# Kernel optimization log

Hardware: AMD Instinct MI355X
Metric: run time of the kernel (lower is better)

The kernel has to match this reference:

```python
import jax, jax.numpy as jnp
import numpy as np

EPS = 1e-5

def _conv1x1_bn(x, W, b, g, beta):
    # 1x1 conv == channel matmul; BN in training mode uses batch stats over (N,H,W)
    y = jnp.einsum('bchw,oc->bohw', x, W) + b[None, :, None, None]
    mu = jnp.mean(y, axis=(0, 2, 3))
    var = jnp.var(y, axis=(0, 2, 3))
    y = (y - mu[None, :, None, None]) * jax.lax.rsqrt(var + EPS)[None, :, None, None]
    return y * g[None, :, None, None] + beta[None, :, None, None]


def setup_inputs() -> dict:
    key = jax.random.key(0)
    ks = jax.random.split(key, 7)
    b, c, h, w = 8, 256, 64, 64
    sc = 1.0 / np.sqrt(c)
    inp = {
        'x': jax.random.normal(ks[0], (b, c, h, w), jnp.float32),
        'Wq': jax.random.normal(ks[1], (c, c), jnp.float32) * sc,
        'bq': jax.random.normal(ks[2], (c,), jnp.float32) * 0.02,
        'gq': jnp.ones((c,), jnp.float32),
        'betaq': jnp.zeros((c,), jnp.float32),
        'Wk': jax.random.normal(ks[3], (c, c), jnp.float32) * sc,
        'bk': jax.random.normal(ks[4], (c,), jnp.float32) * 0.02,
        'gk': jnp.ones((c,), jnp.float32),
        'betak': jnp.zeros((c,), jnp.float32),
        'Wv': jax.random.normal(ks[5], (c, c), jnp.float32) * sc,
        'bv': jax.random.normal(ks[6], (c,), jnp.float32) * 0.02,
        'gv': jnp.ones((c,), jnp.float32),
        'betav': jnp.zeros((c,), jnp.float32),
    }
    return inp


def reference(x, Wq, bq, gq, betaq, Wk, bk, gk, betak, Wv, bv, gv, betav):
    b, c, h, w = x.shape
    scale = float(h) ** (-0.5)
    Q = _conv1x1_bn(x, Wq, bq, gq, betaq).reshape(b, c, h * w)
    K = _conv1x1_bn(x, Wk, bk, gk, betak).reshape(b, c, h * w)
    V = _conv1x1_bn(x, Wv, bv, gv, betav).reshape(b, c, h * w)
    # un-normalized attention (no softmax)
    pixelMap = jnp.einsum('bcq,bck->bqk', Q, K) * scale  # [b, N, N]
    out = jnp.einsum('bqk,bck->bcq', pixelMap, V)        # [b, c, N]
    return out.reshape(b, c, h, w)
```

## Files before the change

### kernel.cpp

```cpp
#include <hip/hip_runtime.h>
#include <hip/hip_bf16.h>


#define BB 8
#define CC 256
#define NPIX 4096
#define PTOT 32768
#define EPSV 1e-5f
#define SCALEV 0.125f

#define OFF_PG    0L
#define OFF_SP    6291456L
#define OFF_S     6324224L
#define OFF_GHAT  6326272L
#define OFF_XBAR  6391808L
#define OFF_WP    6392064L
#define OFF_WKTF  6588672L
#define OFF_WVTF  6654208L
#define OFF_CVEC  6719744L
#define OFF_U     6720512L
#define OFF_HB    6722560L
#define OFF_R     6724608L
#define OFF_OFFV  6724864L
#define OFF_GBF   6726912L
#define OFF_WQT   6989056L
#define OFF_WKT   7021824L
#define OFF_WVB   7054592L
#define OFF_ZT    7087360L
#define OFF_TBF   7120128L

typedef __attribute__((ext_vector_type(8))) short short8;
typedef __attribute__((ext_vector_type(4))) float f32x4;

#define MFMA16(a, b, c) __builtin_amdgcn_mfma_f32_16x16x32_bf16((a), (b), (c), 0, 0, 0)

__device__ __forceinline__ ushort f2bf(float f) {
    union { float f; unsigned u; } v; v.f = f;
    const unsigned r = (v.u + 0x7FFFu + ((v.u >> 16) & 1u)) >> 16;
    return (ushort)r;
}

__device__ __forceinline__ float bf2f(ushort u) {
    union { unsigned u; float f; } v; v.u = ((unsigned)u) << 16;
    return v.f;
}

__device__ __forceinline__ ushort2 f2bf2(float a, float b) {
    __hip_bfloat162 h = __float22bfloat162_rn(float2{a, b});
    union { __hip_bfloat162 h; ushort2 u; } v; v.h = h;
    return v.u;
}

__device__ __forceinline__ float block_reduce(float v, float* red, int tid) {
    red[tid] = v; __syncthreads();
    for (int st = 128; st > 0; st >>= 1) {
        if (tid < st) red[tid] += red[tid + st];
        __syncthreads();
    }
    float r = red[0]; __syncthreads();
    return r;
}

__device__ __forceinline__ float2 wred2(float a, float b, float* red8, int tid) {
    #pragma unroll
    for (int s = 32; s > 0; s >>= 1) {
        a += __shfl_xor(a, s);
        b += __shfl_xor(b, s);
    }
    if ((tid & 63) == 0) { red8[(tid >> 6) * 2] = a; red8[(tid >> 6) * 2 + 1] = b; }
    __syncthreads();
    const float ra = red8[0] + red8[2] + red8[4] + red8[6];
    const float rb = red8[1] + red8[3] + red8[5] + red8[7];
    __syncthreads();
    return float2{ra, rb};
}

__global__ __launch_bounds__(256, 2) void gram_mfma(const float* __restrict__ x,
                                                    float* __restrict__ Pg,
                                                    float* __restrict__ Sp,
                                                    float* __restrict__ Ghat) {
    __shared__ __align__(16) ushort Ab[128 * 72];
    __shared__ __align__(16) ushort Bb[128 * 72];
    __shared__ float rs[128];
    const int tid = threadIdx.x;
    const int ks = blockIdx.x, b = blockIdx.y, tt = blockIdx.z;
    const int lb = (tt * 8 + b) * 16 + ks;
    if (lb < 64) {
        #pragma unroll
        for (int i = 0; i < 4; ++i) Ghat[lb * 1024 + i * 256 + tid] = 0.f;
    }
    const int it = (tt == 1) ? 1 : 0;
    const int jt = (tt == 0) ? 0 : 1;
    const bool diag = (tt < 2);
    const int i0 = it * 128, j0 = jt * 128, k0 = ks * 256;
    const float* xb = x + (long)b * CC * NPIX;
    const int c = tid & 15, rp = tid >> 4;
    const int wave = tid >> 6, lane = tid & 63;
    const int wr = (wave >> 1) * 64, wc = (wave & 1) * 64;
    const int m = lane & 15, q8 = (lane >> 4) * 8;

    if (tid < 128) rs[tid] = 0.f;
    float rloc[8] = {};
    f32x4 acc[4][4];
    #pragma unroll
    for (int a = 0; a < 4; ++a)
        #pragma unroll
        for (int q = 0; q < 4; ++q) acc[a][q] = (f32x4){0.f, 0.f, 0.f, 0.f};

    const float* Abase = xb + (long)i0 * NPIX + k0 + c * 4;
    const float* Bbase = xb + (long)j0 * NPIX + k0 + c * 4;

    float4 va[8], vb[8];
    #pragma unroll
    for (int pp = 0; pp < 8; ++pp)
        va[pp] = *(const float4*)&Abase[(long)(pp * 16 + rp) * NPIX];
    if (!diag) {
        #pragma unroll
        for (int pp = 0; pp < 8; ++pp)
            vb[pp] = *(const float4*)&Bbase[(long)(pp * 16 + rp) * NPIX];
    }

    for (int kc = 0; kc < 256; kc += 64) {
        __syncthreads();
        #pragma unroll
        for (int pp = 0; pp < 8; ++pp) {
            const int row = pp * 16 + rp;
            const float4 v = va[pp];
            rloc[pp] += v.x + v.y + v.z + v.w;
            const ushort2 w01 = f2bf2(v.x, v.y);
            const ushort2 w23 = f2bf2(v.z, v.w);
            ushort4 w; w.x = w01.x; w.y = w01.y; w.z = w23.x; w.w = w23.y;
            *(ushort4*)&Ab[row * 72 + c * 4] = w;
        }
        if (!diag) {
            #pragma unroll
            for (int pp = 0; pp < 8; ++pp) {
                const int row = pp * 16 + rp;
                const float4 v = vb[pp];
                const ushort2 w01 = f2bf2(v.x, v.y);
                const ushort2 w23 = f2bf2(v.z, v.w);
                ushort4 w; w.x = w01.x; w.y = w01.y; w.z = w23.x; w.w = w23.y;
                *(ushort4*)&Bb[row * 72 + c * 4] = w;
            }
        }
        const int kn = kc + 64;
        if (kn < 256) {
            #pragma unroll
            for (int pp = 0; pp < 8; ++pp)
                va[pp] = *(const float4*)&Abase[(long)(pp * 16 + rp) * NPIX + kn];
            if (!diag) {
                #pragma unroll
                for (int pp = 0; pp < 8; ++pp)
                    vb[pp] = *(const float4*)&Bbase[(long)(pp * 16 + rp) * NPIX + kn];
            }
        }
        __syncthreads();
        const ushort* Bsrc = diag ? Ab : Bb;
        #pragma unroll
        for (int kk = 0; kk < 2; ++kk) {
            short8 af[4], bfv[4];
            #pragma unroll
            for (int a = 0; a < 4; ++a)
                af[a] = *(const short8*)&Ab[(wr + a * 16 + m) * 72 + kk * 32 + q8];
            #pragma unroll
            for (int q = 0; q < 4; ++q)
                bfv[q] = *(const short8*)&Bsrc[(wc + q * 16 + m) * 72 + kk * 32 + q8];
            #pragma unroll
            for (int a = 0; a < 4; ++a)
                #pragma unroll
                for (int q = 0; q < 4; ++q)
                    acc[a][q] = MFMA16(af[a], bfv[q], acc[a][q]);
        }
    }
    if (diag) {
        #pragma unroll
        for (int pp = 0; pp < 8; ++pp) atomicAdd(&rs[pp * 16 + rp], rloc[pp]);
        __syncthreads();
        if (tid < 128) Sp[(((long)ks * 8 + b) * 2 + it) * 128 + tid] = rs[tid];
    }
    float* Pt = Pg + (((long)ks * 8 + b) * 3 + tt) * 16384;
    const int rq = (lane >> 4) * 4;
    #pragma unroll
    for (int a = 0; a < 4; ++a) {
        #pragma unroll
        for (int q = 0; q < 4; ++q) {
            const int col = wc + q * 16 + m;
            #pragma unroll
            for (int reg = 0; reg < 4; ++reg)
                Pt[(long)(wr + a * 16 + rq + reg) * 128 + col] = acc[a][q][reg];
        }
    }
}

__global__ __launch_bounds__(256) void reduce_mirror(const float* __restrict__ Pg,
                                                     const float* __restrict__ Sp,
                                                     ushort* __restrict__ Gbf,
                                                     float* __restrict__ Ghat,
                                                     float* __restrict__ S,
                                                     float* __restrict__ xbar) {
    const int blk = blockIdx.x, tid = threadIdx.x;
    if (blk == 384) {
        const int it2 = tid >> 7, rr = tid & 127;
        float xacc = 0.f;
        for (int b = 0; b < BB; ++b) {
            float acc = 0.f;
            #pragma unroll
            for (int ks = 0; ks < 16; ++ks)
                acc += Sp[(((long)ks * 8 + b) * 2 + it2) * 128 + rr];
            S[b * 256 + tid] = acc;
            xacc += acc;
        }
        xbar[tid] = xacc * (1.0f / PTOT);
        return;
    }
    __shared__ float tile[32][33];
    const int tt = blk >> 7;
    const int sub = (blk >> 3) & 15;
    const int b = blk & 7;
    const int sr = (sub >> 2) * 32, sc = (sub & 3) * 32;
    const int it = (tt == 1) ? 1 : 0;
    const int jt = (tt == 0) ? 0 : 1;
    const bool offd = (tt == 2);
    const int gi0 = it * 128 + sr, gj0 = jt * 128 + sc;
    const int r = tid >> 3, c4 = (tid & 7) * 4;
    const float inv = 1.0f / PTOT;

    float s0 = 0.f, s1 = 0.f, s2 = 0.f, s3 = 0.f;
    #pragma unroll
    for (int ks = 0; ks < 16; ++ks) {
        const float4 v = *(const float4*)&Pg[(((long)ks * 8 + b) * 3 + tt) * 16384
                                             + (long)(sr + r) * 128 + sc + c4];
        s0 += v.x; s1 += v.y; s2 += v.z; s3 += v.w;
    }
    ushort4 w;
    w.x = f2bf(s0); w.y = f2bf(s1); w.z = f2bf(s2); w.w = f2bf(s3);
    *(ushort4*)&Gbf[(long)b * 65536 + (long)(gi0 + r) * 256 + gj0 + c4] = w;
    float* gd = &Ghat[(long)(gi0 + r) * 256 + gj0 + c4];
    atomicAdd(gd + 0, s0 * inv);
    atomicAdd(gd + 1, s1 * inv);
    atomicAdd(gd + 2, s2 * inv);
    atomicAdd(gd + 3, s3 * inv);
    if (offd) {
        tile[r][c4 + 0] = s0; tile[r][c4 + 1] = s1;
        tile[r][c4 + 2] = s2; tile[r][c4 + 3] = s3;
        __syncthreads();
        const float t0 = tile[c4 + 0][r], t1 = tile[c4 + 1][r];
        const float t2 = tile[c4 + 2][r], t3 = tile[c4 + 3][r];
        ushort4 tw;
        tw.x = f2bf(t0); tw.y = f2bf(t1); tw.z = f2bf(t2); tw.w = f2bf(t3);
        *(ushort4*)&Gbf[(long)b * 65536 + (long)(gj0 + r) * 256 + gi0 + c4] = tw;
        float* gm = &Ghat[(long)(gj0 + r) * 256 + gi0 + c4];
        atomicAdd(gm + 0, t0 * inv);
        atomicAdd(gm + 1, t1 * inv);
        atomicAdd(gm + 2, t2 * inv);
        atomicAdd(gm + 3, t3 * inv);
    }
}

__global__ __launch_bounds__(256) void stats_quad(const float* __restrict__ Wq, const float* __restrict__ Wk,
                           const float* __restrict__ Wv, const float* __restrict__ Ghat,
                           const float* __restrict__ xbar,
                           const float* bq, const float* gq, const float* betaq,
                           const float* bk, const float* gk, const float* betak,
                           const float* bv, const float* gv, const float* betav,
                           float* __restrict__ Wp, float* __restrict__ cvec,
                           ushort* __restrict__ WqT, ushort* __restrict__ WkT,
                           ushort* __restrict__ Wvb, float* __restrict__ WkTf,
                           float* __restrict__ WvTf) {
    const int og = blockIdx.x, t = blockIdx.y, tid = threadIdx.x;
    const int o0 = og * 4;
    const float* Wt  = t == 0 ? Wq : (t == 1 ? Wk : Wv);
    const float* bt  = t == 0 ? bq : (t == 1 ? bk : bv);
    const float* gt  = t == 0 ? gq : (t == 1 ? gk : gv);
    const float* bet = t == 0 ? betaq : (t == 1 ? betak : betav);
    __shared__ float wrows[4][256];
    __shared__ float red8[8];
    #pragma unroll
    for (int i = 0; i < 4; ++i) wrows[i][tid] = Wt[(o0 + i) * 256 + tid];
    const float xb = xbar[tid];
    __syncthreads();
    const float* grow = Ghat + (long)tid * 256;
    float tj[4] = {0.f, 0.f, 0.f, 0.f};
    #pragma unroll 8
    for (int k = 0; k < 256; k += 4) {
        const float4 g = *(const float4*)&grow[k];
        #pragma unroll
        for (int i = 0; i < 4; ++i)
            tj[i] += g.x * wrows[i][k]     + g.y * wrows[i][k + 1]
                   + g.z * wrows[i][k + 2] + g.w * wrows[i][k + 3];
    }
    #pragma unroll
    for (int i = 0; i < 4; ++i) {
        const int o = o0 + i;
        const float wv = wrows[i][tid];
        const float2 qw = wred2(wv * tj[i], wv * xb, red8, tid);
        const float bo = bt[o];
        const float mu = qw.y + bo;
        const float var = qw.x + 2.f * bo * mu - bo * bo - mu * mu;
        const float a = gt[o] * rsqrtf(var + EPSV);
        const float wpv = a * wv;
        Wp[(long)t * 65536 + o * 256 + tid] = wpv;
        const ushort wb = f2bf(wpv);
        if (t == 0) {
            WqT[(long)tid * 256 + o] = wb;
        } else if (t == 1) {
            WkT[(long)tid * 256 + o] = wb;
            WkTf[(long)tid * 256 + o] = wpv;
        } else {
            Wvb[(long)o * 256 + tid] = wb;
            WvTf[(long)tid * 256 + o] = wpv;
        }
        if (tid == 0) cvec[t * 256 + o] = a * (bo - mu) + bet[o];
    }
}

__device__ __forceinline__ void gemm_tile0(const ushort* __restrict__ Ab,
                                           const ushort* __restrict__ Bb,
                                           ushort* __restrict__ Db,
                                           int m0, int n0, int tid) {
    const int wave = tid >> 6, lane = tid & 63;
    const int wr = (wave >> 1) * 64, wc = (wave & 1) * 64;
    const int m = lane & 15, q8 = (lane >> 4) * 8;
    f32x4 acc[4][4];
    #pragma unroll
    for (int a = 0; a < 4; ++a)
        #pragma unroll
        for (int q = 0; q < 4; ++q) acc[a][q] = (f32x4){0.f, 0.f, 0.f, 0.f};
    #pragma unroll
    for (int kk = 0; kk < 8; ++kk) {
        short8 af[4], bfv[4];
        #pragma unroll
        for (int a = 0; a < 4; ++a)
            af[a] = *(const short8*)&Ab[(long)(m0 + wr + a * 16 + m) * 256 + kk * 32 + q8];
        #pragma unroll
        for (int q = 0; q < 4; ++q)
            bfv[q] = *(const short8*)&Bb[(long)(n0 + wc + q * 16 + m) * 256 + kk * 32 + q8];
        #pragma unroll
        for (int a = 0; a < 4; ++a)
            #pragma unroll
            for (int q = 0; q < 4; ++q)
                acc[a][q] = MFMA16(af[a], bfv[q], acc[a][q]);
    }
    const int rq = (lane >> 4) * 4;
    #pragma unroll
    for (int a = 0; a < 4; ++a) {
        #pragma unroll
        for (int q = 0; q < 4; ++q) {
            const int col = n0 + wc + q * 16 + m;
            #pragma unroll
            for (int reg = 0; reg < 4; ++reg)
                Db[(long)col * 256 + (m0 + wr + a * 16 + rq + reg)] = f2bf(acc[a][q][reg]);
        }
    }
}

__global__ __launch_bounds__(256) void zmidabc(const ushort* __restrict__ WkT,
                                               const ushort* __restrict__ WqT,
                                               ushort* __restrict__ ZT,
                                               const float* __restrict__ Wp,
                                               const float* __restrict__ WkTf,
                                               const float* __restrict__ WvTf,
                                               const float* __restrict__ S,
                                               const float* __restrict__ cvec,
                                               const ushort* __restrict__ Gbf,
                                               float* __restrict__ u,
                                               float* __restrict__ hb,
                                               float* __restrict__ r_,
                                               float* __restrict__ offv) {
    const int blk = blockIdx.x, tid = threadIdx.x;
    if (blk < 4) {
        gemm_tile0(WkT, WqT, ZT, (blk >> 1) * 128, (blk & 1) * 128, tid);
        return;
    }
    const int b = blk - 4;
    __shared__ float sh[256], wl[256], yl[256], red[256], cqs[256], cks[256];
    sh[tid]  = S[b * 256 + tid];
    cqs[tid] = cvec[tid];
    cks[tid] = cvec[256 + tid];
    __syncthreads();
    float uu = 0.f, ww = 0.f, yy = 0.f, rr = 0.f;
    #pragma unroll 8
    for (int j = 0; j < 256; ++j) {
        const float sv = sh[j];
        uu += WvTf[(long)j * 256 + tid] * sv;
        ww += WkTf[(long)j * 256 + tid] * sv;
    }
    #pragma unroll 8
    for (int o = 0; o < 256; ++o) {
        yy += Wp[65536L + (long)o * 256 + tid] * cqs[o];
        rr += Wp[(long)o * 256 + tid] * cks[o];
    }
    u[b * 256 + tid] = uu;
    if (b == 0) r_[tid] = rr;
    wl[tid] = ww; yl[tid] = yy;
    __syncthreads();
    float hh = 0.f, gg = 0.f;
    #pragma unroll 8
    for (int o = 0; o < 256; ++o) {
        hh += Wp[(long)o * 256 + tid] * wl[o];
        gg += bf2f(Gbf[(long)b * 65536 + (long)o * 256 + tid]) * yl[o];
    }
    hb[b * 256 + tid] = hh;
    __syncthreads();
    sh[tid] = gg;
    __syncthreads();
    float vg = 0.f;
    #pragma unroll 8
    for (int j = 0; j < 256; ++j) vg += WvTf[(long)j * 256 + tid] * sh[j];
    const float cv = cvec[512 + tid];
    const float dkq = block_reduce(cqs[tid] * cks[tid], red, tid);
    const float dwq = block_reduce(wl[tid] * cqs[tid], red, tid);
    offv[b * 256 + tid] = SCALEV * (vg + uu * dkq + cv * (dwq + 4096.0f * dkq));
}

__global__ __launch_bounds__(256, 2) void gemm_FT(const ushort* __restrict__ Gbf,
                                                  const ushort* __restrict__ ZT,
                                                  const ushort* __restrict__ Wvb,
                                                  ushort* __restrict__ Tbf,
                                                  const float* __restrict__ u,
                                                  const float* __restrict__ cvec,
                                                  const float* __restrict__ r_,
                                                  const float* __restrict__ hb) {
    __shared__ __align__(16) ushort zt[64 * 256];
    const int blk = blockIdx.x, tid = threadIdx.x;
    const int b = blk >> 2, j0 = (blk & 3) * 64;
    const int wave = tid >> 6, lane = tid & 63;
    const int m = lane & 15, qq = lane >> 4;
    const int q8 = qq * 8;
    f32x4 acc[4][4];

    #pragma unroll
    for (int a = 0; a < 4; ++a)
        #pragma unroll
        for (int q = 0; q < 4; ++q) acc[a][q] = (f32x4){0.f, 0.f, 0.f, 0.f};
    const ushort* Gb = Gbf + (long)b * 65536;
    const ushort* Zs = ZT + (long)j0 * 256;
    #pragma unroll
    for (int kk = 0; kk < 8; ++kk) {
        short8 af[4], bv[4];
        #pragma unroll
        for (int a = 0; a < 4; ++a)
            af[a] = *(const short8*)&Gb[(long)(wave * 64 + a * 16 + m) * 256 + kk * 32 + q8];
        #pragma unroll
        for (int q = 0; q < 4; ++q)
            bv[q] = *(const short8*)&Zs[(long)(q * 16 + m) * 256 + kk * 32 + q8];
        #pragma unroll
        for (int a = 0; a < 4; ++a)
            #pragma unroll
            for (int q = 0; q < 4; ++q)
                acc[a][q] = MFMA16(af[a], bv[q], acc[a][q]);
    }
    #pragma unroll
    for (int a = 0; a < 4; ++a)
        #pragma unroll
        for (int q = 0; q < 4; ++q) {
            const int col = q * 16 + m;
            const int rowb = wave * 64 + a * 16 + qq * 4;
            const ushort2 p01 = f2bf2(acc[a][q][0], acc[a][q][1]);
            const ushort2 p23 = f2bf2(acc[a][q][2], acc[a][q][3]);
            ushort4 w4; w4.x = p01.x; w4.y = p01.y; w4.z = p23.x; w4.w = p23.y;
            *(ushort4*)&zt[col * 256 + (rowb ^ ((col & 7) << 3))] = w4;
        }
    __syncthreads();

    #pragma unroll
    for (int a = 0; a < 4; ++a)
        #pragma unroll
        for (int q = 0; q < 4; ++q) acc[a][q] = (f32x4){0.f, 0.f, 0.f, 0.f};
    #pragma unroll
    for (int kk = 0; kk < 8; ++kk) {
        short8 af[4], bv[4];
        #pragma unroll
        for (int a = 0; a < 4; ++a)
            af[a] = *(const short8*)&Wvb[(long)(wave * 64 + a * 16 + m) * 256 + kk * 32 + q8];
        #pragma unroll
        for (int q = 0; q < 4; ++q) {
            const int col = q * 16 + m;
            bv[q] = *(const short8*)&zt[col * 256 + ((kk * 32 + q8) ^ ((col & 7) << 3))];
        }
        #pragma unroll
        for (int a = 0; a < 4; ++a)
            #pragma unroll
            for (int q = 0; q < 4; ++q)
                acc[a][q] = MFMA16(af[a], bv[q], acc[a][q]);
    }
    const int rq4 = qq * 4;
    #pragma unroll
    for (int a = 0; a < 4; ++a) {
        #pragma unroll
        for (int q = 0; q < 4; ++q) {
            const int cg = j0 + q * 16 + m;
            const float rv = r_[cg];
            const float t2 = hb[b * 256 + cg] + 4096.0f * rv;
            #pragma unroll
            for (int reg = 0; reg < 4; ++reg) {
                const int row = wave * 64 + a * 16 + rq4 + reg;
                const float val = SCALEV * (acc[a][q][reg] + u[b * 256 + row] * rv
                                            + cvec[512 + row] * t2);
                Tbf[(long)b * 65536 + (long)row * 256 + cg] = f2bf(val);
            }
        }
    }
}

__global__ __launch_bounds__(256) void out_mfma(const ushort* __restrict__ Tbf,
                                                const float* __restrict__ x,
                                                const float* __restrict__ offv,
                                                float* __restrict__ out) {
    __shared__ __align__(16) ushort Bs[64 * 264];
    const int tid = threadIdx.x;
    const int p0 = blockIdx.x * 64;
    const int b = blockIdx.y;
    const float* xb = x + (long)b * CC * NPIX;
    const ushort* Tb = Tbf + (long)b * 65536;

    const int c = tid & 15, kq = tid >> 4;
    #pragma unroll
    for (int kt = 0; kt < 4; ++kt) {
        const int k4 = kt * 64 + kq * 4;
        const int p = c * 4;
        const float4 v0 = *(const float4*)&xb[(long)(k4 + 0) * NPIX + p0 + p];
        const float4 v1 = *(const float4*)&xb[(long)(k4 + 1) * NPIX + p0 + p];
        const float4 v2 = *(const float4*)&xb[(long)(k4 + 2) * NPIX + p0 + p];
        const float4 v3 = *(const float4*)&xb[(long)(k4 + 3) * NPIX + p0 + p];
        ushort2 a01, a23;
        ushort4 w;
        a01 = f2bf2(v0.x, v1.x); a23 = f2bf2(v2.x, v3.x);
        w.x = a01.x; w.y = a01.y; w.z = a23.x; w.w = a23.y;
        *(ushort4*)&Bs[(p + 0) * 264 + k4] = w;
        a01 = f2bf2(v0.y, v1.y); a23 = f2bf2(v2.y, v3.y);
        w.x = a01.x; w.y = a01.y; w.z = a23.x; w.w = a23.y;
        *(ushort4*)&Bs[(p + 1) * 264 + k4] = w;
        a01 = f2bf2(v0.z, v1.z); a23 = f2bf2(v2.z, v3.z);
        w.x = a01.x; w.y = a01.y; w.z = a23.x; w.w = a23.y;
        *(ushort4*)&Bs[(p + 2) * 264 + k4] = w;
        a01 = f2bf2(v0.w, v1.w); a23 = f2bf2(v2.w, v3.w);
        w.x = a01.x; w.y = a01.y; w.z = a23.x; w.w = a23.y;
        *(ushort4*)&Bs[(p + 3) * 264 + k4] = w;
    }
    __syncthreads();

    const int wave = tid >> 6, lane = tid & 63;
    const int wr = wave * 64;
    const int m = lane & 15, q8 = (lane >> 4) * 8;
    f32x4 acc[4][4];
    #pragma unroll
    for (int a = 0; a < 4; ++a)
        #pragma unroll
        for (int q = 0; q < 4; ++q) acc[a][q] = (f32x4){0.f, 0.f, 0.f, 0.f};

    #pragma unroll
    for (int kk = 0; kk < 8; ++kk) {
        short8 af[4], bfv[4];
        #pragma unroll
        for (int a = 0; a < 4; ++a)
            af[a] = *(const short8*)&Tb[(long)(wr + a * 16 + m) * 256 + kk * 32 + q8];
        #pragma unroll
        for (int q = 0; q < 4; ++q)
            bfv[q] = *(const short8*)&Bs[(q * 16 + m) * 264 + kk * 32 + q8];
        #pragma unroll
        for (int a = 0; a < 4; ++a)
            #pragma unroll
            for (int q = 0; q < 4; ++q)
                acc[a][q] = MFMA16(af[a], bfv[q], acc[a][q]);
    }

    const int rq = (lane >> 4) * 4;
    #pragma unroll
    for (int a = 0; a < 4; ++a) {
        #pragma unroll
        for (int reg = 0; reg < 4; ++reg) {
            const int row = wr + a * 16 + rq + reg;
            const float off_ = offv[b * CC + row];
            float* orow = &out[((long)b * CC + row) * NPIX + p0];
            #pragma unroll
            for (int q = 0; q < 4; ++q)
                orow[q * 16 + m] = acc[a][q][reg] + off_;
        }
    }
}

extern "C" void kernel_launch(void* const* d_in, const int* in_sizes, int n_in,
                              void* d_out, int out_size, void* d_ws, size_t ws_size,
                              hipStream_t stream) {
    const float* x     = (const float*)d_in[0];
    const float* Wq    = (const float*)d_in[1];
    const float* bq    = (const float*)d_in[2];
    const float* gq    = (const float*)d_in[3];
    const float* betaq = (const float*)d_in[4];
    const float* Wk    = (const float*)d_in[5];
    const float* bk    = (const float*)d_in[6];
    const float* gk    = (const float*)d_in[7];
    const float* betak = (const float*)d_in[8];
    const float* Wv    = (const float*)d_in[9];
    const float* bv    = (const float*)d_in[10];
    const float* gv    = (const float*)d_in[11];
    const float* betav = (const float*)d_in[12];
    float* ws = (float*)d_ws;

    float*  Pg   = ws + OFF_PG;
    float*  Sp   = ws + OFF_SP;
    float*  S    = ws + OFF_S;
    float*  Ghat = ws + OFF_GHAT;
    float*  Xbar = ws + OFF_XBAR;
    float*  Wp   = ws + OFF_WP;
    float*  WkTf = ws + OFF_WKTF;
    float*  WvTf = ws + OFF_WVTF;
    float*  cvec = ws + OFF_CVEC;
    float*  U    = ws + OFF_U;
    float*  Hb   = ws + OFF_HB;
    float*  R    = ws + OFF_R;
    float*  OffV = ws + OFF_OFFV;
    ushort* Gbf  = (ushort*)(ws + OFF_GBF);
    ushort* WqT  = (ushort*)(ws + OFF_WQT);
    ushort* WkT  = (ushort*)(ws + OFF_WKT);
    ushort* Wvb  = (ushort*)(ws + OFF_WVB);
    ushort* ZT   = (ushort*)(ws + OFF_ZT);
    ushort* Tbf  = (ushort*)(ws + OFF_TBF);

    gram_mfma<<<dim3(16, 8, 3), 256, 0, stream>>>(x, Pg, Sp, Ghat);
    reduce_mirror<<<385, 256, 0, stream>>>(Pg, Sp, Gbf, Ghat, S, Xbar);
    stats_quad<<<dim3(64, 3), 256, 0, stream>>>(Wq, Wk, Wv, Ghat, Xbar,
                                                bq, gq, betaq, bk, gk, betak,
                                                bv, gv, betav, Wp, cvec,
                                                WqT, WkT, Wvb, WkTf, WvTf);
    zmidabc<<<12, 256, 0, stream>>>(WkT, WqT, ZT, Wp, WkTf, WvTf, S, cvec, Gbf,
                                    U, Hb, R, OffV);
    gemm_FT<<<32, 256, 0, stream>>>(Gbf, ZT, Wvb, Tbf, U, cvec, R, Hb);
    out_mfma<<<dim3(64, 8), 256, 0, stream>>>(Tbf, x, OffV, (float*)d_out);
}
```

Baseline: 217.4 us.

## Split serial small-vector stages across more blocks with atomic accumulation

The 12-block zmidabc kernel ran long serial 256-step matrix-vector loops per batch. This change splits those loops into 64-row chunks spread over many blocks that accumulate with atomicAdd into a zeroed accumulator buffer. The fused 32-block gemm_FT, which did two chained GEMMs in shared memory, becomes two kernels: bcF2 computes G·Z into a new FT buffer and tvg computes Wv·F. The offset vector is now computed in the out_mfma epilogue. This adds one kernel launch, atomic traffic and order-dependent float rounding in exchange for much more parallelism on the small dependent stages.

Result: faster. 190.1 us, median of 2 (-12.6%).

```diff
diff --git a/kernel.cpp b/kernel.cpp
--- a/kernel.cpp
+++ b/kernel.cpp
@@ -18,16 +18,24 @@
 #define OFF_WKTF  6588672L
 #define OFF_WVTF  6654208L
 #define OFF_CVEC  6719744L
-#define OFF_U     6720512L
-#define OFF_HB    6722560L
-#define OFF_R     6724608L
-#define OFF_OFFV  6724864L
-#define OFF_GBF   6726912L
-#define OFF_WQT   6989056L
-#define OFF_WKT   7021824L
-#define OFF_WVB   7054592L
-#define OFF_ZT    7087360L
-#define OFF_TBF   7120128L
+#define OFF_ACC   6720512L
+#define OFF_GBF   6732800L
+#define OFF_WQT   6994944L
+#define OFF_WKT   7027712L
+#define OFF_WVB   7060480L
+#define OFF_ZT    7093248L
+#define OFF_FT    7126016L
+#define OFF_TBF   7388160L
+
+#define ACC_U    0
+#define ACC_W    2048
+#define ACC_Y    4096
+#define ACC_R    4352
+#define ACC_H    4608
+#define ACC_G    6656
+#define ACC_VG   8704
+#define ACC_SCAL 10752
+#define ACC_TOT  12288
 
 typedef __attribute__((ext_vector_type(8))) short short8;
 typedef __attribute__((ext_vector_type(4))) float f32x4;
@@ -78,7 +86,8 @@
 __global__ __launch_bounds__(256, 2) void gram_mfma(const float* __restrict__ x,
                                                     float* __restrict__ Pg,
                                                     float* __restrict__ Sp,
-                                                    float* __restrict__ Ghat) {
+                                                    float* __restrict__ Ghat,
+                                                    float* __restrict__ Acc) {
     __shared__ __align__(16) ushort Ab[128 * 72];
     __shared__ __align__(16) ushort Bb[128 * 72];
     __shared__ float rs[128];
@@ -88,6 +97,10 @@
     if (lb < 64) {
         #pragma unroll
         for (int i = 0; i < 4; ++i) Ghat[lb * 1024 + i * 256 + tid] = 0.f;
+    } else if (lb < 76) {
+        const int base = (lb - 64) * 1024;
+        #pragma unroll
+        for (int i = 0; i < 4; ++i) Acc[base + i * 256 + tid] = 0.f;
     }
     const int it = (tt == 1) ? 1 : 0;
     const int jt = (tt == 0) ? 0 : 1;
@@ -354,158 +367,162 @@
     }
 }
 
-__global__ __launch_bounds__(256) void zmidabc(const ushort* __restrict__ WkT,
-                                               const ushort* __restrict__ WqT,
-                                               ushort* __restrict__ ZT,
-                                               const float* __restrict__ Wp,
-                                               const float* __restrict__ WkTf,
-                                               const float* __restrict__ WvTf,
-                                               const float* __restrict__ S,
-                                               const float* __restrict__ cvec,
-                                               const ushort* __restrict__ Gbf,
-                                               float* __restrict__ u,
-                                               float* __restrict__ hb,
-                                               float* __restrict__ r_,
-                                               float* __restrict__ offv) {
+__global__ __launch_bounds__(256) void zmida(const ushort* __restrict__ WkT,
+                                             const ushort* __restrict__ WqT,
+                                             ushort* __restrict__ ZT,
+                                             const float* __restrict__ Wp,
+                                             const float* __restrict__ WkTf,
+                                             const float* __restrict__ WvTf,
+                                             const float* __restrict__ S,
+                                             const float* __restrict__ cvec,
+                                             float* __restrict__ Acc) {
     const int blk = blockIdx.x, tid = threadIdx.x;
+    __shared__ float sa[64], sb[64];
     if (blk < 4) {
         gemm_tile0(WkT, WqT, ZT, (blk >> 1) * 128, (blk & 1) * 128, tid);
         return;
     }
-    const int b = blk - 4;
-    __shared__ float sh[256], wl[256], yl[256], red[256], cqs[256], cks[256];
-    sh[tid]  = S[b * 256 + tid];
-    cqs[tid] = cvec[tid];
-    cks[tid] = cvec[256 + tid];
-    __syncthreads();
-    float uu = 0.f, ww = 0.f, yy = 0.f, rr = 0.f;
-    #pragma unroll 8
-    for (int j = 0; j < 256; ++j) {
-        const float sv = sh[j];
-        uu += WvTf[(long)j * 256 + tid] * sv;
-        ww += WkTf[(long)j * 256 + tid] * sv;
-    }
-    #pragma unroll 8
-    for (int o = 0; o < 256; ++o) {
-        yy += Wp[65536L + (long)o * 256 + tid] * cqs[o];
-        rr += Wp[(long)o * 256 + tid] * cks[o];
-    }
-    u[b * 256 + tid] = uu;
-    if (b == 0) r_[tid] = rr;
-    wl[tid] = ww; yl[tid] = yy;
-    __syncthreads();
-    float hh = 0.f, gg = 0.f;
-    #pragma unroll 8
-    for (int o = 0; o < 256; ++o) {
-        hh += Wp[(long)o * 256 + tid] * wl[o];
-        gg += bf2f(Gbf[(long)b * 65536 + (long)o * 256 + tid]) * yl[o];
-    }
-    hb[b * 256 + tid] = hh;
-    __syncthreads();
-    sh[tid] = gg;
-    __syncthreads();
-    float vg = 0.f;
-    #pragma unroll 8
-    for (int j = 0; j < 256; ++j) vg += WvTf[(long)j * 256 + tid] * sh[j];
-    const float cv = cvec[512 + tid];
-    const float dkq = block_reduce(cqs[tid] * cks[tid], red, tid);
-    const float dwq = block_reduce(wl[tid] * cqs[tid], red, tid);
-    offv[b * 256 + tid] = SCALEV * (vg + uu * dkq + cv * (dwq + 4096.0f * dkq));
-}
-
-__global__ __launch_bounds__(256, 2) void gemm_FT(const ushort* __restrict__ Gbf,
-                                                  const ushort* __restrict__ ZT,
-                                                  const ushort* __restrict__ Wvb,
-                                                  ushort* __restrict__ Tbf,
-                                                  const float* __restrict__ u,
-                                                  const float* __restrict__ cvec,
-                                                  const float* __restrict__ r_,
-                                                  const float* __restrict__ hb) {
-    __shared__ __align__(16) ushort zt[64 * 256];
+    if (blk < 36) {
+        const int b = (blk - 4) >> 2, j0 = ((blk - 4) & 3) * 64;
+        if (tid < 64) sa[tid] = S[b * 256 + j0 + tid];
+        __syncthreads();
+        float uu = 0.f, ww = 0.f;
+        #pragma unroll 8
+        for (int i = 0; i < 64; ++i) {
+            const float sv = sa[i];
+            uu += WvTf[(long)(j0 + i) * 256 + tid] * sv;
+            ww += WkTf[(long)(j0 + i) * 256 + tid] * sv;
+        }
+        atomicAdd(&Acc[ACC_U + b * 256 + tid], uu);
+        atomicAdd(&Acc[ACC_W + b * 256 + tid], ww);
+    } else {
+        const int o0 = (blk - 36) * 64;
+        if (tid < 64) { sa[tid] = cvec[o0 + tid]; sb[tid] = cvec[256 + o0 + tid]; }
+        __syncthreads();
+        float yy = 0.f, rr = 0.f;
+        #pragma unroll 8
+        for (int i = 0; i < 64; ++i) {
+            yy += Wp[65536L + (long)(o0 + i) * 256 + tid] * sa[i];
+            rr += Wp[(long)(o0 + i) * 256 + tid] * sb[i];
+        }
+        atomicAdd(&Acc[ACC_Y + tid], yy);
+        atomicAdd(&Acc[ACC_R + tid], rr);
+    }
+}
+
+__global__ __launch_bounds__(256) void bcF2(const ushort* __restrict__ Gbf,
+                                            const ushort* __restrict__ ZT,
+                                            ushort* __restrict__ FT,
+                                            const float* __restrict__ Wp,
+                                            const float* __restrict__ cvec,
+                                            float* __restrict__ Acc) {
     const int blk = blockIdx.x, tid = threadIdx.x;
-    const int b = blk >> 2, j0 = (blk & 3) * 64;
-    const int wave = tid >> 6, lane = tid & 63;
-    const int m = lane & 15, qq = lane >> 4;
-    const int q8 = qq * 8;
-    f32x4 acc[4][4];
-
-    #pragma unroll
-    for (int a = 0; a < 4; ++a)
-        #pragma unroll
-        for (int q = 0; q < 4; ++q) acc[a][q] = (f32x4){0.f, 0.f, 0.f, 0.f};
-    const ushort* Gb = Gbf + (long)b * 65536;
-    const ushort* Zs = ZT + (long)j0 * 256;
-    #pragma unroll
-    for (int kk = 0; kk < 8; ++kk) {
-        short8 af[4], bv[4];
+    __shared__ float sa[64];
+    __shared__ float red[256];
+    if (blk < 32) {
+        const int bz = blk >> 2, t = blk & 3;
+        gemm_tile0(Gbf + (long)bz * 65536, ZT, FT + (long)bz * 65536,
+                   (t >> 1) * 128, (t & 1) * 128, tid);
+        return;
+    }
+    if (blk < 64) {
+        const int b = (blk - 32) >> 2, o0 = ((blk - 32) & 3) * 64;
+        if (tid < 64) sa[tid] = Acc[ACC_W + b * 256 + o0 + tid];
+        __syncthreads();
+        float hh = 0.f;
+        #pragma unroll 8
+        for (int i = 0; i < 64; ++i)
+            hh += Wp[(long)(o0 + i) * 256 + tid] * sa[i];
+        atomicAdd(&Acc[ACC_H + b * 256 + tid], hh);
+    } else if (blk < 96) {
+        const int b = (blk - 64) >> 2, o0 = ((blk - 64) & 3) * 64;
+        if (tid < 64) sa[tid] = Acc[ACC_Y + o0 + tid];
+        __syncthreads();
+        float gg = 0.f;
+        #pragma unroll 8
+        for (int i = 0; i < 64; ++i)
+            gg += bf2f(Gbf[(long)b * 65536 + (long)(o0 + i) * 256 + tid]) * sa[i];
+        atomicAdd(&Acc[ACC_G + b * 256 + tid], gg);
+    } else {
+        const float cq = cvec[tid], ck = cvec[256 + tid];
+        const float dkq = block_reduce(cq * ck, red, tid);
+        if (tid == 0) Acc[ACC_SCAL] = dkq;
+        for (int b = 0; b < BB; ++b) {
+            const float dwq = block_reduce(Acc[ACC_W + b * 256 + tid] * cq, red, tid);
+            if (tid == 0) Acc[ACC_SCAL + 1 + b] = dwq;
+        }
+    }
+}
+
+__global__ __launch_bounds__(256) void tvg(const ushort* __restrict__ Wvb,
+                                           const ushort* __restrict__ FT,
+                                           ushort* __restrict__ Tbf,
+                                           const float* __restrict__ WvTf,
+                                           const float* __restrict__ cvec,
+                                           float* __restrict__ Acc) {
+    const int blk = blockIdx.x, tid = threadIdx.x;
+    __shared__ float sa[64];
+    if (blk < 32) {
+        const int bz = blk >> 2, t = blk & 3;
+        const int m0 = (t >> 1) * 128, n0 = (t & 1) * 128;
+        const ushort* Fb = FT + (long)bz * 65536;
+        const int wave = tid >> 6, lane = tid & 63;
+        const int wr = (wave >> 1) * 64, wc = (wave & 1) * 64;
+        const int m = lane & 15, q8 = (lane >> 4) * 8;
+        f32x4 acc[4][4];
         #pragma unroll
         for (int a = 0; a < 4; ++a)
-            af[a] = *(const short8*)&Gb[(long)(wave * 64 + a * 16 + m) * 256 + kk * 32 + q8];
-        #pragma unroll
-        for (int q = 0; q < 4; ++q)
-            bv[q] = *(const short8*)&Zs[(long)(q * 16 + m) * 256 + kk * 32 + q8];
-        #pragma unroll
-        for (int a = 0; a < 4; ++a)
+            #pragma unroll
+            for (int q = 0; q < 4; ++q) acc[a][q] = (f32x4){0.f, 0.f, 0.f, 0.f};
+        #pragma unroll
+        for (int kk = 0; kk < 8; ++kk) {
+            short8 af[4], bfv[4];
+            #pragma unroll
+            for (int a = 0; a < 4; ++a)
+                af[a] = *(const short8*)&Wvb[(long)(m0 + wr + a * 16 + m) * 256 + kk * 32 + q8];
             #pragma unroll
             for (int q = 0; q < 4; ++q)
-                acc[a][q] = MFMA16(af[a], bv[q], acc[a][q]);
-    }
-    #pragma unroll
-    for (int a = 0; a < 4; ++a)
-        #pragma unroll
-        for (int q = 0; q < 4; ++q) {
-            const int col = q * 16 + m;
-            const int rowb = wave * 64 + a * 16 + qq * 4;
-            const ushort2 p01 = f2bf2(acc[a][q][0], acc[a][q][1]);
-            const ushort2 p23 = f2bf2(acc[a][q][2], acc[a][q][3]);
-            ushort4 w4; w4.x = p01.x; w4.y = p01.y; w4.z = p23.x; w4.w = p23.y;
-            *(ushort4*)&zt[col * 256 + (rowb ^ ((col & 7) << 3))] = w4;
-        }
-    __syncthreads();
-
-    #pragma unroll
-    for (int a = 0; a < 4; ++a)
-        #pragma unroll
-        for (int q = 0; q < 4; ++q) acc[a][q] = (f32x4){0.f, 0.f, 0.f, 0.f};
-    #pragma unroll
-    for (int kk = 0; kk < 8; ++kk) {
-        short8 af[4], bv[4];
-        #pragma unroll
-        for (int a = 0; a < 4; ++a)
-            af[a] = *(const short8*)&Wvb[(long)(wave * 64 + a * 16 + m) * 256 + kk * 32 + q8];
-        #pragma unroll
-        for (int q = 0; q < 4; ++q) {
-            const int col = q * 16 + m;
-            bv[q] = *(const short8*)&zt[col * 256 + ((kk * 32 + q8) ^ ((col & 7) << 3))];
-        }
-        #pragma unroll
-        for (int a = 0; a < 4; ++a)
-            #pragma unroll
-            for (int q = 0; q < 4; ++q)
-                acc[a][q] = MFMA16(af[a], bv[q], acc[a][q]);
-    }
-    const int rq4 = qq * 4;
-    #pragma unroll
-    for (int a = 0; a < 4; ++a) {
-        #pragma unroll
-        for (int q = 0; q < 4; ++q) {
-            const int cg = j0 + q * 16 + m;
-            const float rv = r_[cg];
-            const float t2 = hb[b * 256 + cg] + 4096.0f * rv;
-            #pragma unroll
-            for (int reg = 0; reg < 4; ++reg) {
-                const int row = wave * 64 + a * 16 + rq4 + reg;
-                const float val = SCALEV * (acc[a][q][reg] + u[b * 256 + row] * rv
-                                            + cvec[512 + row] * t2);
-                Tbf[(long)b * 65536 + (long)row * 256 + cg] = f2bf(val);
+                bfv[q] = *(const short8*)&Fb[(long)(n0 + wc + q * 16 + m) * 256 + kk * 32 + q8];
+            #pragma unroll
+            for (int a = 0; a < 4; ++a)
+                #pragma unroll
+                for (int q = 0; q < 4; ++q)
+                    acc[a][q] = MFMA16(af[a], bfv[q], acc[a][q]);
+        }
+        const int rq = (lane >> 4) * 4;
+        #pragma unroll
+        for (int a = 0; a < 4; ++a) {
+            #pragma unroll
+            for (int q = 0; q < 4; ++q) {
+                const int col = n0 + wc + q * 16 + m;
+                const float rv = Acc[ACC_R + col];
+                const float t2 = Acc[ACC_H + bz * 256 + col] + 4096.0f * rv;
+                #pragma unroll
+                for (int reg = 0; reg < 4; ++reg) {
+                    const int row = m0 + wr + a * 16 + rq + reg;
+                    const float val = SCALEV * (acc[a][q][reg]
+                                                + Acc[ACC_U + bz * 256 + row] * rv
+                                                + cvec[512 + row] * t2);
+                    Tbf[(long)bz * 65536 + (long)row * 256 + col] = f2bf(val);
+                }
             }
         }
+    } else {
+        const int b = (blk - 32) >> 2, j0 = ((blk - 32) & 3) * 64;
+        if (tid < 64) sa[tid] = Acc[ACC_G + b * 256 + j0 + tid];
+        __syncthreads();
+        float vg = 0.f;
+        #pragma unroll 8
+        for (int i = 0; i < 64; ++i)
+            vg += WvTf[(long)(j0 + i) * 256 + tid] * sa[i];
+        atomicAdd(&Acc[ACC_VG + b * 256 + tid], vg);
     }
 }
 
 __global__ __launch_bounds__(256) void out_mfma(const ushort* __restrict__ Tbf,
                                                 const float* __restrict__ x,
-                                                const float* __restrict__ offv,
+                                                const float* __restrict__ Acc,
+                                                const float* __restrict__ cvec,
                                                 float* __restrict__ out) {
     __shared__ __align__(16) ushort Bs[64 * 264];
     const int tid = threadIdx.x;
@@ -513,6 +530,8 @@
     const int b = blockIdx.y;
     const float* xb = x + (long)b * CC * NPIX;
     const ushort* Tb = Tbf + (long)b * 65536;
+    const float dkq = Acc[ACC_SCAL];
+    const float dwqb = Acc[ACC_SCAL + 1 + b];
 
     const int c = tid & 15, kq = tid >> 4;
     #pragma unroll
@@ -571,7 +590,9 @@
         #pragma unroll
         for (int reg = 0; reg < 4; ++reg) {
             const int row = wr + a * 16 + rq + reg;
-            const float off_ = offv[b * CC + row];
+            const float off_ = SCALEV * (Acc[ACC_VG + b * 256 + row]
+                                         + Acc[ACC_U + b * 256 + row] * dkq
+                                         + cvec[512 + row] * (dwqb + 4096.0f * dkq));
             float* orow = &out[((long)b * CC + row) * NPIX + p0];
             #pragma unroll
             for (int q = 0; q < 4; ++q)
@@ -607,25 +628,23 @@
     float*  WkTf = ws + OFF_WKTF;
     float*  WvTf = ws + OFF_WVTF;
     float*  cvec = ws + OFF_CVEC;
-    float*  U    = ws + OFF_U;
-    float*  Hb   = ws + OFF_HB;
-    float*  R    = ws + OFF_R;
-    float*  OffV = ws + OFF_OFFV;
+    float*  Acc  = ws + OFF_ACC;
     ushort* Gbf  = (ushort*)(ws + OFF_GBF);
     ushort* WqT  = (ushort*)(ws + OFF_WQT);
     ushort* WkT  = (ushort*)(ws + OFF_WKT);
     ushort* Wvb  = (ushort*)(ws + OFF_WVB);
     ushort* ZT   = (ushort*)(ws + OFF_ZT);
+    ushort* FT   = (ushort*)(ws + OFF_FT);
     ushort* Tbf  = (ushort*)(ws + OFF_TBF);
 
-    gram_mfma<<<dim3(16, 8, 3), 256, 0, stream>>>(x, Pg, Sp, Ghat);
+    gram_mfma<<<dim3(16, 8, 3), 256, 0, stream>>>(x, Pg, Sp, Ghat, Acc);
     reduce_mirror<<<385, 256, 0, stream>>>(Pg, Sp, Gbf, Ghat, S, Xbar);
     stats_quad<<<dim3(64, 3), 256, 0, stream>>>(Wq, Wk, Wv, Ghat, Xbar,
                                                 bq, gq, betaq, bk, gk, betak,
                                                 bv, gv, betav, Wp, cvec,
                                                 WqT, WkT, Wvb, WkTf, WvTf);
-    zmidabc<<<12, 256, 0, stream>>>(WkT, WqT, ZT, Wp, WkTf, WvTf, S, cvec, Gbf,
-                                    U, Hb, R, OffV);
-    gemm_FT<<<32, 256, 0, stream>>>(Gbf, ZT, Wvb, Tbf, U, cvec, R, Hb);
-    out_mfma<<<dim3(64, 8), 256, 0, stream>>>(Tbf, x, OffV, (float*)d_out);
-}
+    zmida<<<40, 256, 0, stream>>>(WkT, WqT, ZT, Wp, WkTf, WvTf, S, cvec, Acc);
+    bcF2<<<97, 256, 0, stream>>>(Gbf, ZT, FT, Wp, cvec, Acc);
+    tvg<<<64, 256, 0, stream>>>(Wvb, FT, Tbf, WvTf, cvec, Acc);
+    out_mfma<<<dim3(64, 8), 256, 0, stream>>>(Tbf, x, Acc, cvec, (float*)d_out);
+}
```
